# Performance work log

Measured on AMD Instinct MI355X. Metric: run time of the kernel, lower is better.

Reference implementation:

```python
import jax, jax.numpy as jnp
import numpy as np
import math

H, G, DQK, DV = 16, 4, 64, 128  # n_head, n_kv_group, qk head dim, v head dim


def _rope(t):
    # t: [B, n, T, d] -- standard rotate-half RoPE, base 10000
    B, n, T, d = t.shape
    inv = 1.0 / (10000.0 ** (jnp.arange(0, d, 2, dtype=jnp.float32) / d))  # [d/2]
    ang = jnp.arange(T, dtype=jnp.float32)[:, None] * inv[None, :]          # [T, d/2]
    cos = jnp.concatenate([jnp.cos(ang), jnp.cos(ang)], axis=-1)            # [T, d]
    sin = jnp.concatenate([jnp.sin(ang), jnp.sin(ang)], axis=-1)
    t1, t2 = jnp.split(t, 2, axis=-1)
    rot = jnp.concatenate([-t2, t1], axis=-1)
    return t * cos + rot * sin


def setup_inputs() -> dict:
    key = jax.random.key(0)
    ks = jax.random.split(key, 6)
    B, T, C = 2, 2048, 1024
    x = jax.random.normal(ks[0], (B, T, C), jnp.float32)
    Wq = jax.random.normal(ks[1], (C, H * DQK), jnp.float32) * 0.02
    Wk = jax.random.normal(ks[2], (C, G * DQK), jnp.float32) * 0.02
    Wv = jax.random.normal(ks[3], (C, G * DV), jnp.float32) * 0.02
    Wproj = jax.random.normal(ks[4], (DV, C), jnp.float32) * 0.02
    lobo = jnp.full((H,), 1.0, jnp.float32)  # flash_lobo_log_const per head
    g0 = math.log2(T * T - T)                # qk_norm_factor init from block_size
    qk_norm_factor = jnp.array([g0], dtype=jnp.float32)
    return {"x": x, "iter_num": 0, "Wq": Wq, "Wk": Wk, "Wv": Wv,
            "Wproj": Wproj, "lobo": lobo, "qk_norm_factor": qk_norm_factor}


def reference(x, iter_num, Wq, Wk, Wv, Wproj, lobo, qk_norm_factor):
    B, T, C = x.shape
    # projections (bias=False)
    q = (x @ Wq).reshape(B, T, H, DQK).transpose(0, 2, 1, 3)   # [B,H,T,dqk]
    k = (x @ Wk).reshape(B, T, G, DQK).transpose(0, 2, 1, 3)   # [B,G,T,dqk]
    v = (x @ Wv).reshape(B, T, G, DV).transpose(0, 2, 1, 3)    # [B,G,T,dv]
    # rotary embeddings on q and k
    q = _rope(q)
    k = _rope(k)
    # qk-norm
    q = q / (jnp.linalg.norm(q, axis=-1, keepdims=True) + 1e-6)
    k = k / (jnp.linalg.norm(k, axis=-1, keepdims=True) + 1e-6)
    # learned logit scale: q *= g*sqrt(d), SDPA divides by sqrt(d) -> net scale g
    q = q * (qk_norm_factor[0] * jnp.sqrt(jnp.float32(DQK)))
    # GQA broadcast (repeat_interleave over kv groups)
    rep = H // G
    k = jnp.repeat(k, rep, axis=1)   # [B,H,T,dqk]
    v = jnp.repeat(v, rep, axis=1)   # [B,H,T,dv]
    logits = jnp.einsum('bhqd,bhkd->bhqk', q, k) / jnp.sqrt(jnp.float32(DQK))
    causal = jnp.tril(jnp.ones((T, T), dtype=bool))
    logits = jnp.where(causal[None, None], logits, -jnp.inf)
    # flash-lobo: zero-valued sink key, always visible, logit = per-head bias
    sink = jnp.broadcast_to(lobo[None, :, None, None], (B, H, T, 1))
    att = jax.nn.softmax(jnp.concatenate([sink, logits], axis=-1), axis=-1)
    y = jnp.einsum('bhqk,bhkd->bhqd', att[..., 1:], v)  # sink value is zero
    y = y.sum(axis=1)                                    # head-SUM merge [B,T,dv]
    return y @ Wproj                                     # [B,T,C]
```

## Files before the change

### kernel.cpp

```cpp
#include <hip/hip_runtime.h>
#include <hip/hip_bf16.h>
#include <math.h>

#define B_ 2
#define T_ 2048
#define C_ 1024
#define H_ 16
#define G_ 4
#define DQK_ 64
#define DV_ 128
#define NQKV 1792
#define KS2 2048

typedef __attribute__((ext_vector_type(8))) short short8;
typedef __attribute__((ext_vector_type(4))) float f32x4;
typedef unsigned short ushort_t;

__device__ inline ushort_t f2bf(float f) {
  union { float f; unsigned int u; } v; v.f = f;
  unsigned int r = (v.u + 0x7FFFu + ((v.u >> 16) & 1u)) >> 16;
  return (ushort_t)r;
}
__device__ inline float bf2f(ushort_t h) {
  union { unsigned int u; float f; } v; v.u = ((unsigned int)h) << 16;
  return v.f;
}
__device__ inline ushort_t f2bf_hw(float f) {
  unsigned int u;
  asm("v_cvt_pk_bf16_f32 %0, %1, %1" : "=v"(u) : "v"(f));
  return (ushort_t)u;
}

#define GLD_LDS16(g, l)                                              \
  __builtin_amdgcn_global_load_lds(                                  \
      (const __attribute__((address_space(1))) void*)(g),            \
      (__attribute__((address_space(3))) void*)(l), 16, 0, 0)

__global__ __launch_bounds__(256) void cast_x(
    const float* __restrict__ x, ushort_t* __restrict__ xb) {
  int idx = blockIdx.x * 256 + threadIdx.x;
  int m = idx >> 7;
  int c8 = idx & 127;
  const float* src = &x[(size_t)m * 1024 + c8 * 8];
  float4 v0 = *(const float4*)&src[0];
  float4 v1 = *(const float4*)&src[4];
  float f[8] = {v0.x, v0.y, v0.z, v0.w, v1.x, v1.y, v1.z, v1.w};
  short8 hv, lv;
#pragma unroll
  for (int c = 0; c < 8; c++) {
    ushort_t h = f2bf(f[c]);
    hv[c] = (short)h;
    lv[c] = (short)f2bf(f[c] - bf2f(h));
  }
  int key = (m >> 1) & 3;
  int phys = (c8 & ~3) * 8 + ((c8 & 3) ^ key) * 8;
  ushort_t* row = xb + (size_t)m * KS2;
  *(short8*)&row[phys] = hv;
  *(short8*)&row[1024 + phys] = lv;
}

__global__ __launch_bounds__(256) void cast_w(
    const float* __restrict__ Wq, const float* __restrict__ Wk,
    const float* __restrict__ Wv, ushort_t* __restrict__ wt) {
  __shared__ float tile[64][65];
  const int n0 = blockIdx.x * 64;
  const int k0 = blockIdx.y * 64;
  const int tid = threadIdx.x;

  const float* Wp; int ldw, noff;
  if (n0 < 1024)      { Wp = Wq; ldw = 1024; noff = n0; }
  else if (n0 < 1280) { Wp = Wk; ldw = 256;  noff = n0 - 1024; }
  else                { Wp = Wv; ldw = 512;  noff = n0 - 1280; }

#pragma unroll
  for (int it = 0; it < 4; it++) {
    int fi = it * 256 + tid;
    int kk = fi >> 4;
    int nc = (fi & 15) * 4;
    float4 v = *(const float4*)&Wp[(size_t)(k0 + kk) * ldw + noff + nc];
    tile[nc + 0][kk] = v.x; tile[nc + 1][kk] = v.y;
    tile[nc + 2][kk] = v.z; tile[nc + 3][kk] = v.w;
  }
  __syncthreads();
  int nn = tid >> 2, seg = tid & 3;
  int n = n0 + nn;
  int key = (n >> 1) & 3;
  ushort_t* row = wt + (size_t)n * KS2;
#pragma unroll
  for (int j = 0; j < 2; j++) {
    short8 hv;
#pragma unroll
    for (int u = 0; u < 8; u++)
      hv[u] = (short)f2bf(tile[nn][seg * 16 + j * 8 + u]);
    int c8 = (k0 >> 3) + seg * 2 + j;
    int phys = (c8 & ~3) * 8 + ((c8 & 3) ^ key) * 8;
    *(short8*)&row[phys] = hv;
  }
}

__global__ __launch_bounds__(256) void cast_wp(
    const float* __restrict__ Wp, ushort_t* __restrict__ wpf) {
  int idx = blockIdx.x * 256 + threadIdx.x;
  int n = idx & 1023;
  int kc = idx >> 10;
  short8 v;
#pragma unroll
  for (int j = 0; j < 8; j++)
    v[j] = (short)f2bf(Wp[(size_t)(kc * 8 + j) * 1024 + n]);
  size_t off = (((size_t)(n >> 7) * 4 + (kc >> 2)) * 8 + ((n >> 4) & 7)) * 512 +
               ((kc & 3) * 16 + (n & 15)) * 8;
  *(short8*)&wpf[off] = v;
}

__global__ __launch_bounds__(256) void gemm_qkv_mfma(
    const ushort_t* __restrict__ xb, const ushort_t* __restrict__ wt,
    float* __restrict__ qkv) {
  __shared__ ushort_t At[128 * 32];
  __shared__ ushort_t Bt[128 * 32];
  const int tid = threadIdx.x;
  const int wave = tid >> 6, lane = tid & 63;
  const int quad = lane >> 4, l16 = lane & 15;
  const int m0 = blockIdx.y * 128, n0 = blockIdx.x * 128;
  const int wm = (wave & 1) * 64, wn = (wave >> 1) * 64;
  const int physq = (quad ^ ((l16 >> 1) & 3)) * 8;
  const int ntiles = (n0 >= 1280) ? 32 : 64;

  f32x4 acc[4][4];
#pragma unroll
  for (int i = 0; i < 4; i++)
#pragma unroll
    for (int j = 0; j < 4; j++) acc[i][j] = (f32x4){0.f, 0.f, 0.f, 0.f};

  const int rA = wave * 32 + (lane >> 2);
  const int cA = (lane & 3) * 8;
  const ushort_t* gA = xb + (size_t)(m0 + rA) * KS2 + cA;
  const ushort_t* gB = wt + (size_t)(n0 + rA) * KS2 + cA;
  ushort_t* lA0 = At + (size_t)(wave * 32) * 32;
  ushort_t* lA1 = At + (size_t)(wave * 32 + 16) * 32;
  ushort_t* lB0 = Bt + (size_t)(wave * 32) * 32;
  ushort_t* lB1 = Bt + (size_t)(wave * 32 + 16) * 32;

  for (int kt = 0; kt < ntiles; kt++) {
    const int ca = kt * 32;
    const int cb = (kt < 32 ? kt : kt - 32) * 32;
    __syncthreads();
    GLD_LDS16(gA + ca, lA0);
    GLD_LDS16(gA + ca + 16 * KS2, lA1);
    GLD_LDS16(gB + cb, lB0);
    GLD_LDS16(gB + cb + 16 * KS2, lB1);
    __syncthreads();

    short8 af[4], bf[4];
#pragma unroll
    for (int i = 0; i < 4; i++)
      af[i] = *(const short8*)&At[(wm + 16 * i + l16) * 32 + physq];
#pragma unroll
    for (int j = 0; j < 4; j++)
      bf[j] = *(const short8*)&Bt[(wn + 16 * j + l16) * 32 + physq];
#pragma unroll
    for (int i = 0; i < 4; i++)
#pragma unroll
      for (int j = 0; j < 4; j++)
        acc[i][j] = __builtin_amdgcn_mfma_f32_16x16x32_bf16(
            af[i], bf[j], acc[i][j], 0, 0, 0);
  }

#pragma unroll
  for (int i = 0; i < 4; i++) {
    int m = m0 + wm + 16 * i + quad * 4;
#pragma unroll
    for (int j = 0; j < 4; j++) {
      int n = n0 + wn + 16 * j + l16;
#pragma unroll
      for (int r = 0; r < 4; r++)
        qkv[(size_t)(m + r) * NQKV + n] = acc[i][j][r];
    }
  }
}

__global__ __launch_bounds__(256) void rope_norm(
    const float* __restrict__ qkv,
    ushort_t* __restrict__ qf, ushort_t* __restrict__ kf) {
  const int NQ = B_ * T_ * H_;
  int vec = blockIdx.x * 4 + (threadIdx.x >> 6);
  int d = threadIdx.x & 63;

  size_t src; int t, b, isq; ushort_t* dstbase;
  if (vec < NQ) {
    int h = vec % H_; int bt = vec / H_;
    t = bt % T_; b = bt / T_;
    src = (size_t)bt * NQKV + h * 64 + d;
    dstbase = qf + (size_t)(b * 16 + h) * 131072;
    isq = 1;
  } else {
    int vk = vec - NQ;
    int g = vk % G_; int bt = vk / G_;
    t = bt % T_; b = bt / T_;
    src = (size_t)bt * NQKV + 1024 + g * 64 + d;
    dstbase = kf + (size_t)(b * 4 + g) * 131072;
    isq = 0;
  }
  float val = qkv[src];
  int i = d & 31;
  float inv = exp2f(-(float)i * 0.4152410118074239f);
  float ang = (float)t * inv;
  float sn, cs;
  __sincosf(ang, &sn, &cs);
  float partner = __shfl(val, d ^ 32, 64);
  float r = (d < 32) ? (val * cs - partner * sn) : (val * cs + partner * sn);
  float ss = r * r;
#pragma unroll
  for (int off = 32; off; off >>= 1) ss += __shfl_xor(ss, off, 64);
  r *= 1.0f / (sqrtf(ss) + 1e-6f);

  int kt = t >> 6, tt = t & 63;
  int l16v = tt & 15;
  int ks = d >> 5, quad = (d >> 3) & 3, j = d & 7;
  size_t off2;
  if (isq) {
    int wavei = tt >> 4;
    off2 = ((size_t)(kt * 8 + wavei * 2 + ks) * 4 + quad) * 128 + l16v * 8 + j;
  } else {
    int nt = tt >> 4;
    off2 = ((size_t)(kt * 8 + ks * 4 + nt) * 4 + quad) * 128 + l16v * 8 + j;
  }
  dstbase[off2] = f2bf(r);
}

__global__ __launch_bounds__(256) void vscatter(
    const float* __restrict__ qkv, ushort_t* __restrict__ vf) {
  int idx = blockIdx.x * 256 + threadIdx.x;
  int dv = idx & 127;
  int t = (idx >> 7) & 2047;
  int g = (idx >> 18) & 3;
  int b = idx >> 20;
  size_t src = (size_t)(b * T_ + t) * NQKV + 1280 + g * 128 + dv;
  float v = qkv[src];
  int kt = t >> 6, ks = (t >> 5) & 1, quad = (t >> 3) & 3, j = t & 7;
  int nv = dv >> 4, l16v = dv & 15;
  size_t off = ((size_t)(kt * 16 + ks * 8 + nv) * 4 + quad) * 128 + l16v * 8 + j;
  vf[(size_t)(b * 4 + g) * 262144 + off] = f2bf(v);
}

__global__ __launch_bounds__(256, 4) void attn(
    const ushort_t* __restrict__ qf, const ushort_t* __restrict__ kf,
    const ushort_t* __restrict__ vf, const float* __restrict__ lobo,
    const float* __restrict__ qknf, float* __restrict__ y) {
  const int f = blockIdx.x;
  const int bh = f & 31;
  const int slot = f >> 5;
  int tq;
  if (slot < 8)       tq = 31 - slot;
  else if (slot < 16) tq = 8 + slot;
  else if (slot < 24) tq = 31 - slot;
  else                tq = slot - 24;
  const int b = bh >> 4;
  const int h = bh & 15;
  const int g = h >> 2;

  __shared__ ushort_t KV[12288];
  __shared__ ushort_t Ps[4 * 1088];

  const int tid = threadIdx.x;
  const int wave = tid >> 6, lane = tid & 63;
  const int quad = lane >> 4, l16 = lane & 15;
  ushort_t* PsW = &Ps[wave * 1088];

  short8 bones;
  {
    short bv = (l16 == 0) ? (short)0x3F80 : (short)0;
#pragma unroll
    for (int j = 0; j < 8; j++) bones[j] = bv;
  }

  const ushort_t* qbase = qf + (size_t)(b * 16 + h) * 131072 + lane * 8;
  short8 aq0 = *(const short8*)&qbase[(size_t)(tq * 8 + wave * 2 + 0) * 512];
  short8 aq1 = *(const short8*)&qbase[(size_t)(tq * 8 + wave * 2 + 1) * 512];

  f32x4 o[9];
#pragma unroll
  for (int nv = 0; nv < 9; nv++) o[nv] = (f32x4){0.f, 0.f, 0.f, 0.f};

  const float gsc = qknf[0];
  const float sinkp = __expf(lobo[h] - gsc);

  const int row = tq * 64 + wave * 16 + quad * 4;

  const ushort_t* kgl = kf + (size_t)(b * 4 + g) * 131072 + lane * 8;
  const ushort_t* vgl = vf + (size_t)(b * 4 + g) * 262144 + lane * 8;

  for (int kt = 0; kt <= tq; kt++) {
    __syncthreads();
    {
      const ushort_t* gk = kgl + (size_t)kt * 4096;
      const ushort_t* gv = vgl + (size_t)kt * 8192;
      GLD_LDS16(gk + (wave * 2 + 0) * 512, &KV[(wave * 2 + 0) * 512]);
      GLD_LDS16(gk + (wave * 2 + 1) * 512, &KV[(wave * 2 + 1) * 512]);
#pragma unroll
      for (int j = 0; j < 4; j++)
        GLD_LDS16(gv + (wave * 4 + j) * 512, &KV[4096 + (wave * 4 + j) * 512]);
    }
    __syncthreads();

    f32x4 s[4];
#pragma unroll
    for (int nt = 0; nt < 4; nt++) s[nt] = (f32x4){0.f, 0.f, 0.f, 0.f};
    {
      short8 kb[4];
#pragma unroll
      for (int u = 0; u < 4; u++)
        kb[u] = *(const short8*)&KV[u * 512 + lane * 8];
      __builtin_amdgcn_s_setprio(1);
#pragma unroll
      for (int nt = 0; nt < 4; nt++)
        s[nt] = __builtin_amdgcn_mfma_f32_16x16x32_bf16(aq0, kb[nt], s[nt], 0, 0, 0);
      __builtin_amdgcn_s_setprio(0);
#pragma unroll
      for (int u = 0; u < 4; u++)
        kb[u] = *(const short8*)&KV[(4 + u) * 512 + lane * 8];
      __builtin_amdgcn_s_setprio(1);
#pragma unroll
      for (int nt = 0; nt < 4; nt++)
        s[nt] = __builtin_amdgcn_mfma_f32_16x16x32_bf16(aq1, kb[nt], s[nt], 0, 0, 0);
      __builtin_amdgcn_s_setprio(0);
    }

    if (kt == tq) {
#pragma unroll
      for (int nt = 0; nt < 4; nt++) {
        int key = kt * 64 + l16 + nt * 16;
#pragma unroll
        for (int r = 0; r < 4; r++) {
          float pv = (key <= row + r) ? __expf(fmaf(s[nt][r], gsc, -gsc)) : 0.f;
          PsW[(quad * 4 + r) * 68 + nt * 16 + l16] = f2bf_hw(pv);
        }
      }
    } else {
#pragma unroll
      for (int nt = 0; nt < 4; nt++)
#pragma unroll
        for (int r = 0; r < 4; r++)
          PsW[(quad * 4 + r) * 68 + nt * 16 + l16] =
              f2bf_hw(__expf(fmaf(s[nt][r], gsc, -gsc)));
    }

    short8 ap0 = *(const short8*)&PsW[l16 * 68 + quad * 8];
    short8 ap1 = *(const short8*)&PsW[l16 * 68 + 32 + quad * 8];
    {
      short8 vb[4];
#pragma unroll
      for (int u = 0; u < 4; u++)
        vb[u] = *(const short8*)&KV[4096 + u * 512 + lane * 8];
      __builtin_amdgcn_s_setprio(1);
#pragma unroll
      for (int nv = 0; nv < 4; nv++)
        o[nv] = __builtin_amdgcn_mfma_f32_16x16x32_bf16(ap0, vb[nv], o[nv], 0, 0, 0);
      __builtin_amdgcn_s_setprio(0);
#pragma unroll
      for (int u = 0; u < 4; u++)
        vb[u] = *(const short8*)&KV[4096 + (4 + u) * 512 + lane * 8];
      __builtin_amdgcn_s_setprio(1);
#pragma unroll
      for (int nv = 0; nv < 4; nv++)
        o[4 + nv] = __builtin_amdgcn_mfma_f32_16x16x32_bf16(ap0, vb[nv], o[4 + nv], 0, 0, 0);
      o[8] = __builtin_amdgcn_mfma_f32_16x16x32_bf16(ap0, bones, o[8], 0, 0, 0);
      o[8] = __builtin_amdgcn_mfma_f32_16x16x32_bf16(ap1, bones, o[8], 0, 0, 0);
      __builtin_amdgcn_s_setprio(0);
#pragma unroll
      for (int u = 0; u < 4; u++)
        vb[u] = *(const short8*)&KV[4096 + (8 + u) * 512 + lane * 8];
      __builtin_amdgcn_s_setprio(1);
#pragma unroll
      for (int nv = 0; nv < 4; nv++)
        o[nv] = __builtin_amdgcn_mfma_f32_16x16x32_bf16(ap1, vb[nv], o[nv], 0, 0, 0);
      __builtin_amdgcn_s_setprio(0);
#pragma unroll
      for (int u = 0; u < 4; u++)
        vb[u] = *(const short8*)&KV[4096 + (12 + u) * 512 + lane * 8];
      __builtin_amdgcn_s_setprio(1);
#pragma unroll
      for (int nv = 0; nv < 4; nv++)
        o[4 + nv] = __builtin_amdgcn_mfma_f32_16x16x32_bf16(ap1, vb[nv], o[4 + nv], 0, 0, 0);
      __builtin_amdgcn_s_setprio(0);
    }
  }

#pragma unroll
  for (int r = 0; r < 4; r++) {
    float lm = __shfl(o[8][r], lane & 48, 64);
    float invl = 1.0f / (lm + sinkp);
    size_t gRow = (size_t)b * T_ + row + r;
#pragma unroll
    for (int nv = 0; nv < 8; nv++)
      atomicAdd(&y[gRow * 128 + nv * 16 + l16], o[nv][r] * invl);
  }
}

__global__ __launch_bounds__(256) void out_proj(
    const float* __restrict__ y, const ushort_t* __restrict__ wpf,
    float* __restrict__ out) {
  __shared__ ushort_t yl[128 * 136];
  const int tid = threadIdx.x;
  const int wave = tid >> 6, lane = tid & 63;
  const int quad = lane >> 4, l16 = lane & 15;
  const int n0 = blockIdx.x * 128, m0 = blockIdx.y * 128;
  const int wm = (wave & 1) * 64, wn = (wave >> 1) * 64;

#pragma unroll
  for (int it = 0; it < 8; it++) {
    int p = it * 256 + tid;
    int row = p >> 4, c8 = p & 15;
    const float* src = &y[(size_t)(m0 + row) * 128 + c8 * 8];
    float4 v0 = *(const float4*)&src[0];
    float4 v1 = *(const float4*)&src[4];
    float fv[8] = {v0.x, v0.y, v0.z, v0.w, v1.x, v1.y, v1.z, v1.w};
    short8 hv;
#pragma unroll
    for (int c = 0; c < 8; c++) hv[c] = (short)f2bf(fv[c]);
    *(short8*)&yl[row * 136 + c8 * 8] = hv;
  }
  __syncthreads();

  f32x4 acc[4][4];
#pragma unroll
  for (int i = 0; i < 4; i++)
#pragma unroll
    for (int j = 0; j < 4; j++) acc[i][j] = (f32x4){0.f, 0.f, 0.f, 0.f};

#pragma unroll
  for (int ks = 0; ks < 4; ks++) {
    short8 af[4], bfr[4];
#pragma unroll
    for (int i = 0; i < 4; i++)
      af[i] = *(const short8*)&yl[(wm + 16 * i + l16) * 136 + (ks * 4 + quad) * 8];
    const ushort_t* wb = wpf + (((size_t)(n0 >> 7) * 4 + ks) * 8) * 512;
#pragma unroll
    for (int j = 0; j < 4; j++)
      bfr[j] = *(const short8*)&wb[((size_t)((wn >> 4) + j)) * 512 + lane * 8];
#pragma unroll
    for (int i = 0; i < 4; i++)
#pragma unroll
      for (int j = 0; j < 4; j++)
        acc[i][j] = __builtin_amdgcn_mfma_f32_16x16x32_bf16(
            af[i], bfr[j], acc[i][j], 0, 0, 0);
  }

#pragma unroll
  for (int i = 0; i < 4; i++) {
    int m = m0 + wm + 16 * i + quad * 4;
#pragma unroll
    for (int j = 0; j < 4; j++) {
      int n = n0 + wn + 16 * j + l16;
#pragma unroll
      for (int r = 0; r < 4; r++)
        out[(size_t)(m + r) * 1024 + n] = acc[i][j][r];
    }
  }
}

extern "C" void kernel_launch(void* const* d_in, const int* in_sizes, int n_in,
                              void* d_out, int out_size, void* d_ws, size_t ws_size,
                              hipStream_t stream) {
  const float* x     = (const float*)d_in[0];
  const float* Wq    = (const float*)d_in[2];
  const float* Wk    = (const float*)d_in[3];
  const float* Wv    = (const float*)d_in[4];
  const float* Wproj = (const float*)d_in[5];
  const float* lobo  = (const float*)d_in[6];
  const float* qknf  = (const float*)d_in[7];
  float* out = (float*)d_out;

  float* qkv = (float*)d_ws;
  ushort_t* xb = (ushort_t*)(qkv + (size_t)B_ * T_ * NQKV);
  ushort_t* wt = xb + (size_t)B_ * T_ * KS2;
  ushort_t* wpf = wt + (size_t)NQKV * KS2;
  ushort_t* qf = xb;
  ushort_t* kf = qf + (size_t)B_ * H_ * T_ * 64;
  ushort_t* vf = kf + (size_t)B_ * G_ * T_ * 64;
  float* y = (float*)(vf + (size_t)B_ * G_ * T_ * 128);

  cast_x<<<(B_ * T_ * 128) / 256, 256, 0, stream>>>(x, xb);
  dim3 gw(NQKV / 64, C_ / 64);
  cast_w<<<gw, 256, 0, stream>>>(Wq, Wk, Wv, wt);
  cast_wp<<<64, 256, 0, stream>>>(Wproj, wpf);

  dim3 gg(NQKV / 128, (B_ * T_) / 128);
  gemm_qkv_mfma<<<gg, 256, 0, stream>>>(xb, wt, qkv);

  int nvec = B_ * T_ * H_ + B_ * T_ * G_;
  rope_norm<<<nvec / 4, 256, 0, stream>>>(qkv, qf, kf);

  vscatter<<<(B_ * G_ * T_ * DV_) / 256, 256, 0, stream>>>(qkv, vf);

  (void)hipMemsetAsync(y, 0, (size_t)B_ * T_ * 128 * sizeof(float), stream);

  attn<<<B_ * H_ * 32, 256, 0, stream>>>(qf, kf, vf, lobo, qknf, y);

  dim3 go(8, 32);
  out_proj<<<go, 256, 0, stream>>>(y, wpf, out);
}
```

Before: 240.6 us.

## Double-buffer K tiles and overlap V loads with QK compute in attention

Splits the shared K/V tile into a double-buffered K buffer and a separate V buffer. Each iteration now issues the V load for the current tile and the K prefetch for the next tile, then runs the QK MFMAs while those loads are in flight, and only waits at a barrier placed before the PV stage. The goal is to hide global-to-LDS load latency behind the score computation. The extra LDS lowers the occupancy hint from 4 to 3 blocks, and the query-tile schedule becomes plain longest-first. The barrier before PV also waits on the next-K prefetch, so the overlap covers only the QK phase.

```diff
diff --git a/kernel.cpp b/kernel.cpp
--- a/kernel.cpp
+++ b/kernel.cpp
@@ -242,23 +242,20 @@
   vf[(size_t)(b * 4 + g) * 262144 + off] = f2bf(v);
 }
 
-__global__ __launch_bounds__(256, 4) void attn(
+__global__ __launch_bounds__(256, 3) void attn(
     const ushort_t* __restrict__ qf, const ushort_t* __restrict__ kf,
     const ushort_t* __restrict__ vf, const float* __restrict__ lobo,
     const float* __restrict__ qknf, float* __restrict__ y) {
   const int f = blockIdx.x;
   const int bh = f & 31;
   const int slot = f >> 5;
-  int tq;
-  if (slot < 8)       tq = 31 - slot;
-  else if (slot < 16) tq = 8 + slot;
-  else if (slot < 24) tq = 31 - slot;
-  else                tq = slot - 24;
+  const int tq = 31 - slot;
   const int b = bh >> 4;
   const int h = bh & 15;
   const int g = h >> 2;
 
-  __shared__ ushort_t KV[12288];
+  __shared__ ushort_t Kb[2][4096];
+  __shared__ ushort_t Vb[8192];
   __shared__ ushort_t Ps[4 * 1088];
 
   const int tid = threadIdx.x;
@@ -289,19 +286,25 @@
   const ushort_t* kgl = kf + (size_t)(b * 4 + g) * 131072 + lane * 8;
   const ushort_t* vgl = vf + (size_t)(b * 4 + g) * 262144 + lane * 8;
 
+  GLD_LDS16(kgl + (wave * 2 + 0) * 512, &Kb[0][(wave * 2 + 0) * 512]);
+  GLD_LDS16(kgl + (wave * 2 + 1) * 512, &Kb[0][(wave * 2 + 1) * 512]);
+  __syncthreads();
+
   for (int kt = 0; kt <= tq; kt++) {
-    __syncthreads();
     {
-      const ushort_t* gk = kgl + (size_t)kt * 4096;
       const ushort_t* gv = vgl + (size_t)kt * 8192;
-      GLD_LDS16(gk + (wave * 2 + 0) * 512, &KV[(wave * 2 + 0) * 512]);
-      GLD_LDS16(gk + (wave * 2 + 1) * 512, &KV[(wave * 2 + 1) * 512]);
 #pragma unroll
       for (int j = 0; j < 4; j++)
-        GLD_LDS16(gv + (wave * 4 + j) * 512, &KV[4096 + (wave * 4 + j) * 512]);
+        GLD_LDS16(gv + (wave * 4 + j) * 512, &Vb[(wave * 4 + j) * 512]);
+      if (kt < tq) {
+        const ushort_t* gk = kgl + (size_t)(kt + 1) * 4096;
+        ushort_t* kd = &Kb[(kt + 1) & 1][0];
+        GLD_LDS16(gk + (wave * 2 + 0) * 512, &kd[(wave * 2 + 0) * 512]);
+        GLD_LDS16(gk + (wave * 2 + 1) * 512, &kd[(wave * 2 + 1) * 512]);
+      }
     }
-    __syncthreads();
-
+
+    const ushort_t* Kc = &Kb[kt & 1][0];
     f32x4 s[4];
 #pragma unroll
     for (int nt = 0; nt < 4; nt++) s[nt] = (f32x4){0.f, 0.f, 0.f, 0.f};
@@ -309,7 +312,7 @@
       short8 kb[4];
 #pragma unroll
       for (int u = 0; u < 4; u++)
-        kb[u] = *(const short8*)&KV[u * 512 + lane * 8];
+        kb[u] = *(const short8*)&Kc[u * 512 + lane * 8];
       __builtin_amdgcn_s_setprio(1);
 #pragma unroll
       for (int nt = 0; nt < 4; nt++)
@@ -317,7 +320,7 @@
       __builtin_amdgcn_s_setprio(0);
 #pragma unroll
       for (int u = 0; u < 4; u++)
-        kb[u] = *(const short8*)&KV[(4 + u) * 512 + lane * 8];
+        kb[u] = *(const short8*)&Kc[(4 + u) * 512 + lane * 8];
       __builtin_amdgcn_s_setprio(1);
 #pragma unroll
       for (int nt = 0; nt < 4; nt++)
@@ -344,13 +347,15 @@
               f2bf_hw(__expf(fmaf(s[nt][r], gsc, -gsc)));
     }
 
+    __syncthreads();
+
     short8 ap0 = *(const short8*)&PsW[l16 * 68 + quad * 8];
     short8 ap1 = *(const short8*)&PsW[l16 * 68 + 32 + quad * 8];
     {
       short8 vb[4];
 #pragma unroll
       for (int u = 0; u < 4; u++)
-        vb[u] = *(const short8*)&KV[4096 + u * 512 + lane * 8];
+        vb[u] = *(const short8*)&Vb[u * 512 + lane * 8];
       __builtin_amdgcn_s_setprio(1);
 #pragma unroll
       for (int nv = 0; nv < 4; nv++)
@@ -358,7 +363,7 @@
       __builtin_amdgcn_s_setprio(0);
 #pragma unroll
       for (int u = 0; u < 4; u++)
-        vb[u] = *(const short8*)&KV[4096 + (4 + u) * 512 + lane * 8];
+        vb[u] = *(const short8*)&Vb[(4 + u) * 512 + lane * 8];
       __builtin_amdgcn_s_setprio(1);
 #pragma unroll
       for (int nv = 0; nv < 4; nv++)
@@ -368,7 +373,7 @@
       __builtin_amdgcn_s_setprio(0);
 #pragma unroll
       for (int u = 0; u < 4; u++)
-        vb[u] = *(const short8*)&KV[4096 + (8 + u) * 512 + lane * 8];
+        vb[u] = *(const short8*)&Vb[(8 + u) * 512 + lane * 8];
       __builtin_amdgcn_s_setprio(1);
 #pragma unroll
       for (int nv = 0; nv < 4; nv++)
@@ -376,13 +381,15 @@
       __builtin_amdgcn_s_setprio(0);
 #pragma unroll
       for (int u = 0; u < 4; u++)
-        vb[u] = *(const short8*)&KV[4096 + (12 + u) * 512 + lane * 8];
+        vb[u] = *(const short8*)&Vb[(12 + u) * 512 + lane * 8];
       __builtin_amdgcn_s_setprio(1);
 #pragma unroll
       for (int nv = 0; nv < 4; nv++)
         o[4 + nv] = __builtin_amdgcn_mfma_f32_16x16x32_bf16(ap1, vb[nv], o[4 + nv], 0, 0, 0);
       __builtin_amdgcn_s_setprio(0);
     }
+
+    __syncthreads();
   }
 
 #pragma unroll
```

Measured after the change: 243.6 us. About the same (+1.2%).

## Merge prep casts and rope/scatter/memset into single launches; widen GEMM K-tile

Applied to the files above, without the earlier changes.

Combines the three weight/activation cast kernels into one block-indexed prep kernel, and the rope-norm, V scatter and y zeroing memset into one rope_scatter kernel. Together this cuts four kernel launches and their inter-kernel gaps. The QKV GEMM now stages 64-wide K tiles per barrier pair instead of 32, using larger LDS buffers. That halves the number of synchronizations per output tile and issues more async loads per barrier. The cost is more shared memory per block and branchy combined kernels.

```diff
diff --git a/kernel.cpp b/kernel.cpp
--- a/kernel.cpp
+++ b/kernel.cpp
@@ -36,94 +36,95 @@
       (const __attribute__((address_space(1))) void*)(g),            \
       (__attribute__((address_space(3))) void*)(l), 16, 0, 0)
 
-__global__ __launch_bounds__(256) void cast_x(
-    const float* __restrict__ x, ushort_t* __restrict__ xb) {
-  int idx = blockIdx.x * 256 + threadIdx.x;
-  int m = idx >> 7;
-  int c8 = idx & 127;
-  const float* src = &x[(size_t)m * 1024 + c8 * 8];
-  float4 v0 = *(const float4*)&src[0];
-  float4 v1 = *(const float4*)&src[4];
-  float f[8] = {v0.x, v0.y, v0.z, v0.w, v1.x, v1.y, v1.z, v1.w};
-  short8 hv, lv;
-#pragma unroll
-  for (int c = 0; c < 8; c++) {
-    ushort_t h = f2bf(f[c]);
-    hv[c] = (short)h;
-    lv[c] = (short)f2bf(f[c] - bf2f(h));
-  }
-  int key = (m >> 1) & 3;
-  int phys = (c8 & ~3) * 8 + ((c8 & 3) ^ key) * 8;
-  ushort_t* row = xb + (size_t)m * KS2;
-  *(short8*)&row[phys] = hv;
-  *(short8*)&row[1024 + phys] = lv;
-}
-
-__global__ __launch_bounds__(256) void cast_w(
-    const float* __restrict__ Wq, const float* __restrict__ Wk,
-    const float* __restrict__ Wv, ushort_t* __restrict__ wt) {
+__global__ __launch_bounds__(256) void prep(
+    const float* __restrict__ x, const float* __restrict__ Wq,
+    const float* __restrict__ Wk, const float* __restrict__ Wv,
+    const float* __restrict__ Wproj, ushort_t* __restrict__ xb,
+    ushort_t* __restrict__ wt, ushort_t* __restrict__ wpf) {
   __shared__ float tile[64][65];
-  const int n0 = blockIdx.x * 64;
-  const int k0 = blockIdx.y * 64;
+  const int bid = blockIdx.x;
   const int tid = threadIdx.x;
 
-  const float* Wp; int ldw, noff;
-  if (n0 < 1024)      { Wp = Wq; ldw = 1024; noff = n0; }
-  else if (n0 < 1280) { Wp = Wk; ldw = 256;  noff = n0 - 1024; }
-  else                { Wp = Wv; ldw = 512;  noff = n0 - 1280; }
-
-#pragma unroll
-  for (int it = 0; it < 4; it++) {
-    int fi = it * 256 + tid;
-    int kk = fi >> 4;
-    int nc = (fi & 15) * 4;
-    float4 v = *(const float4*)&Wp[(size_t)(k0 + kk) * ldw + noff + nc];
-    tile[nc + 0][kk] = v.x; tile[nc + 1][kk] = v.y;
-    tile[nc + 2][kk] = v.z; tile[nc + 3][kk] = v.w;
-  }
-  __syncthreads();
-  int nn = tid >> 2, seg = tid & 3;
-  int n = n0 + nn;
-  int key = (n >> 1) & 3;
-  ushort_t* row = wt + (size_t)n * KS2;
-#pragma unroll
-  for (int j = 0; j < 2; j++) {
-    short8 hv;
-#pragma unroll
-    for (int u = 0; u < 8; u++)
-      hv[u] = (short)f2bf(tile[nn][seg * 16 + j * 8 + u]);
-    int c8 = (k0 >> 3) + seg * 2 + j;
+  if (bid < 2048) {
+    int idx = bid * 256 + tid;
+    int m = idx >> 7;
+    int c8 = idx & 127;
+    const float* src = &x[(size_t)m * 1024 + c8 * 8];
+    float4 v0 = *(const float4*)&src[0];
+    float4 v1 = *(const float4*)&src[4];
+    float f[8] = {v0.x, v0.y, v0.z, v0.w, v1.x, v1.y, v1.z, v1.w};
+    short8 hv, lv;
+#pragma unroll
+    for (int c = 0; c < 8; c++) {
+      ushort_t h = f2bf(f[c]);
+      hv[c] = (short)h;
+      lv[c] = (short)f2bf(f[c] - bf2f(h));
+    }
+    int key = (m >> 1) & 3;
     int phys = (c8 & ~3) * 8 + ((c8 & 3) ^ key) * 8;
+    ushort_t* row = xb + (size_t)m * KS2;
     *(short8*)&row[phys] = hv;
-  }
-}
-
-__global__ __launch_bounds__(256) void cast_wp(
-    const float* __restrict__ Wp, ushort_t* __restrict__ wpf) {
-  int idx = blockIdx.x * 256 + threadIdx.x;
-  int n = idx & 1023;
-  int kc = idx >> 10;
-  short8 v;
-#pragma unroll
-  for (int j = 0; j < 8; j++)
-    v[j] = (short)f2bf(Wp[(size_t)(kc * 8 + j) * 1024 + n]);
-  size_t off = (((size_t)(n >> 7) * 4 + (kc >> 2)) * 8 + ((n >> 4) & 7)) * 512 +
-               ((kc & 3) * 16 + (n & 15)) * 8;
-  *(short8*)&wpf[off] = v;
+    *(short8*)&row[1024 + phys] = lv;
+  } else if (bid < 2496) {
+    const int wid = bid - 2048;
+    const int n0 = (wid % 28) * 64;
+    const int k0 = (wid / 28) * 64;
+
+    const float* Wp; int ldw, noff;
+    if (n0 < 1024)      { Wp = Wq; ldw = 1024; noff = n0; }
+    else if (n0 < 1280) { Wp = Wk; ldw = 256;  noff = n0 - 1024; }
+    else                { Wp = Wv; ldw = 512;  noff = n0 - 1280; }
+
+#pragma unroll
+    for (int it = 0; it < 4; it++) {
+      int fi = it * 256 + tid;
+      int kk = fi >> 4;
+      int nc = (fi & 15) * 4;
+      float4 v = *(const float4*)&Wp[(size_t)(k0 + kk) * ldw + noff + nc];
+      tile[nc + 0][kk] = v.x; tile[nc + 1][kk] = v.y;
+      tile[nc + 2][kk] = v.z; tile[nc + 3][kk] = v.w;
+    }
+    __syncthreads();
+    int nn = tid >> 2, seg = tid & 3;
+    int n = n0 + nn;
+    int key = (n >> 1) & 3;
+    ushort_t* row = wt + (size_t)n * KS2;
+#pragma unroll
+    for (int j = 0; j < 2; j++) {
+      short8 hv;
+#pragma unroll
+      for (int u = 0; u < 8; u++)
+        hv[u] = (short)f2bf(tile[nn][seg * 16 + j * 8 + u]);
+      int c8 = (k0 >> 3) + seg * 2 + j;
+      int phys = (c8 & ~3) * 8 + ((c8 & 3) ^ key) * 8;
+      *(short8*)&row[phys] = hv;
+    }
+  } else {
+    int idx = (bid - 2496) * 256 + tid;
+    int n = idx & 1023;
+    int kc = idx >> 10;
+    short8 v;
+#pragma unroll
+    for (int j = 0; j < 8; j++)
+      v[j] = (short)f2bf(Wproj[(size_t)(kc * 8 + j) * 1024 + n]);
+    size_t off = (((size_t)(n >> 7) * 4 + (kc >> 2)) * 8 + ((n >> 4) & 7)) * 512 +
+                 ((kc & 3) * 16 + (n & 15)) * 8;
+    *(short8*)&wpf[off] = v;
+  }
 }
 
 __global__ __launch_bounds__(256) void gemm_qkv_mfma(
     const ushort_t* __restrict__ xb, const ushort_t* __restrict__ wt,
     float* __restrict__ qkv) {
-  __shared__ ushort_t At[128 * 32];
-  __shared__ ushort_t Bt[128 * 32];
+  __shared__ ushort_t At[128 * 64];
+  __shared__ ushort_t Bt[128 * 64];
   const int tid = threadIdx.x;
   const int wave = tid >> 6, lane = tid & 63;
   const int quad = lane >> 4, l16 = lane & 15;
   const int m0 = blockIdx.y * 128, n0 = blockIdx.x * 128;
   const int wm = (wave & 1) * 64, wn = (wave >> 1) * 64;
-  const int physq = (quad ^ ((l16 >> 1) & 3)) * 8;
-  const int ntiles = (n0 >= 1280) ? 32 : 64;
+  const int key = (l16 >> 1) & 3;
+  const int ntiles = (n0 >= 1280) ? 16 : 32;
 
   f32x4 acc[4][4];
 #pragma unroll
@@ -131,38 +132,39 @@
 #pragma unroll
     for (int j = 0; j < 4; j++) acc[i][j] = (f32x4){0.f, 0.f, 0.f, 0.f};
 
-  const int rA = wave * 32 + (lane >> 2);
-  const int cA = (lane & 3) * 8;
+  const int rA = wave * 32 + (lane >> 3);
+  const int cA = (lane & 7) * 8;
   const ushort_t* gA = xb + (size_t)(m0 + rA) * KS2 + cA;
   const ushort_t* gB = wt + (size_t)(n0 + rA) * KS2 + cA;
-  ushort_t* lA0 = At + (size_t)(wave * 32) * 32;
-  ushort_t* lA1 = At + (size_t)(wave * 32 + 16) * 32;
-  ushort_t* lB0 = Bt + (size_t)(wave * 32) * 32;
-  ushort_t* lB1 = Bt + (size_t)(wave * 32 + 16) * 32;
 
   for (int kt = 0; kt < ntiles; kt++) {
-    const int ca = kt * 32;
-    const int cb = (kt < 32 ? kt : kt - 32) * 32;
+    const int ca = kt * 64;
+    const int cb = (kt < 16 ? kt : kt - 16) * 64;
     __syncthreads();
-    GLD_LDS16(gA + ca, lA0);
-    GLD_LDS16(gA + ca + 16 * KS2, lA1);
-    GLD_LDS16(gB + cb, lB0);
-    GLD_LDS16(gB + cb + 16 * KS2, lB1);
+#pragma unroll
+    for (int j = 0; j < 4; j++) {
+      GLD_LDS16(gA + ca + (size_t)(8 * j) * KS2, &At[(wave * 32 + 8 * j) * 64]);
+      GLD_LDS16(gB + cb + (size_t)(8 * j) * KS2, &Bt[(wave * 32 + 8 * j) * 64]);
+    }
     __syncthreads();
 
-    short8 af[4], bf[4];
-#pragma unroll
-    for (int i = 0; i < 4; i++)
-      af[i] = *(const short8*)&At[(wm + 16 * i + l16) * 32 + physq];
-#pragma unroll
-    for (int j = 0; j < 4; j++)
-      bf[j] = *(const short8*)&Bt[(wn + 16 * j + l16) * 32 + physq];
-#pragma unroll
-    for (int i = 0; i < 4; i++)
+#pragma unroll
+    for (int s = 0; s < 2; s++) {
+      const int off = s * 32 + ((quad ^ key) * 8);
+      short8 af[4], bf[4];
+#pragma unroll
+      for (int i = 0; i < 4; i++)
+        af[i] = *(const short8*)&At[(wm + 16 * i + l16) * 64 + off];
 #pragma unroll
       for (int j = 0; j < 4; j++)
-        acc[i][j] = __builtin_amdgcn_mfma_f32_16x16x32_bf16(
-            af[i], bf[j], acc[i][j], 0, 0, 0);
+        bf[j] = *(const short8*)&Bt[(wn + 16 * j + l16) * 64 + off];
+#pragma unroll
+      for (int i = 0; i < 4; i++)
+#pragma unroll
+        for (int j = 0; j < 4; j++)
+          acc[i][j] = __builtin_amdgcn_mfma_f32_16x16x32_bf16(
+              af[i], bf[j], acc[i][j], 0, 0, 0);
+    }
   }
 
 #pragma unroll
@@ -178,68 +180,74 @@
   }
 }
 
-__global__ __launch_bounds__(256) void rope_norm(
-    const float* __restrict__ qkv,
-    ushort_t* __restrict__ qf, ushort_t* __restrict__ kf) {
-  const int NQ = B_ * T_ * H_;
-  int vec = blockIdx.x * 4 + (threadIdx.x >> 6);
-  int d = threadIdx.x & 63;
-
-  size_t src; int t, b, isq; ushort_t* dstbase;
-  if (vec < NQ) {
-    int h = vec % H_; int bt = vec / H_;
-    t = bt % T_; b = bt / T_;
-    src = (size_t)bt * NQKV + h * 64 + d;
-    dstbase = qf + (size_t)(b * 16 + h) * 131072;
-    isq = 1;
+__global__ __launch_bounds__(256) void rope_scatter(
+    const float* __restrict__ qkv, ushort_t* __restrict__ qf,
+    ushort_t* __restrict__ kf, ushort_t* __restrict__ vf,
+    float* __restrict__ y) {
+  const int bid = blockIdx.x;
+  const int tid = threadIdx.x;
+
+  if (bid < 20480) {
+    const int NQ = B_ * T_ * H_;
+    int vec = bid * 4 + (tid >> 6);
+    int d = tid & 63;
+
+    size_t src; int t, b, isq; ushort_t* dstbase;
+    if (vec < NQ) {
+      int h = vec % H_; int bt = vec / H_;
+      t = bt % T_; b = bt / T_;
+      src = (size_t)bt * NQKV + h * 64 + d;
+      dstbase = qf + (size_t)(b * 16 + h) * 131072;
+      isq = 1;
+    } else {
+      int vk = vec - NQ;
+      int g = vk % G_; int bt = vk / G_;
+      t = bt % T_; b = bt / T_;
+      src = (size_t)bt * NQKV + 1024 + g * 64 + d;
+      dstbase = kf + (size_t)(b * 4 + g) * 131072;
+      isq = 0;
+    }
+    float val = qkv[src];
+    int i = d & 31;
+    float inv = exp2f(-(float)i * 0.4152410118074239f);
+    float ang = (float)t * inv;
+    float sn, cs;
+    __sincosf(ang, &sn, &cs);
+    float partner = __shfl(val, d ^ 32, 64);
+    float r = (d < 32) ? (val * cs - partner * sn) : (val * cs + partner * sn);
+    float ss = r * r;
+#pragma unroll
+    for (int off = 32; off; off >>= 1) ss += __shfl_xor(ss, off, 64);
+    r *= 1.0f / (sqrtf(ss) + 1e-6f);
+
+    int kt = t >> 6, tt = t & 63;
+    int l16v = tt & 15;
+    int ks = d >> 5, quad = (d >> 3) & 3, j = d & 7;
+    size_t off2;
+    if (isq) {
+      int wavei = tt >> 4;
+      off2 = ((size_t)(kt * 8 + wavei * 2 + ks) * 4 + quad) * 128 + l16v * 8 + j;
+    } else {
+      int nt = tt >> 4;
+      off2 = ((size_t)(kt * 8 + ks * 4 + nt) * 4 + quad) * 128 + l16v * 8 + j;
+    }
+    dstbase[off2] = f2bf(r);
+  } else if (bid < 28672) {
+    int idx = (bid - 20480) * 256 + tid;
+    int dv = idx & 127;
+    int t = (idx >> 7) & 2047;
+    int g = (idx >> 18) & 3;
+    int b = idx >> 20;
+    size_t src = (size_t)(b * T_ + t) * NQKV + 1280 + g * 128 + dv;
+    float v = qkv[src];
+    int kt = t >> 6, ks = (t >> 5) & 1, quad = (t >> 3) & 3, j = t & 7;
+    int nv = dv >> 4, l16v = dv & 15;
+    size_t off = ((size_t)(kt * 16 + ks * 8 + nv) * 4 + quad) * 128 + l16v * 8 + j;
+    vf[(size_t)(b * 4 + g) * 262144 + off] = f2bf(v);
   } else {
-    int vk = vec - NQ;
-    int g = vk % G_; int bt = vk / G_;
-    t = bt % T_; b = bt / T_;
-    src = (size_t)bt * NQKV + 1024 + g * 64 + d;
-    dstbase = kf + (size_t)(b * 4 + g) * 131072;
-    isq = 0;
-  }
-  float val = qkv[src];
-  int i = d & 31;
-  float inv = exp2f(-(float)i * 0.4152410118074239f);
-  float ang = (float)t * inv;
-  float sn, cs;
-  __sincosf(ang, &sn, &cs);
-  float partner = __shfl(val, d ^ 32, 64);
-  float r = (d < 32) ? (val * cs - partner * sn) : (val * cs + partner * sn);
-  float ss = r * r;
-#pragma unroll
-  for (int off = 32; off; off >>= 1) ss += __shfl_xor(ss, off, 64);
-  r *= 1.0f / (sqrtf(ss) + 1e-6f);
-
-  int kt = t >> 6, tt = t & 63;
-  int l16v = tt & 15;
-  int ks = d >> 5, quad = (d >> 3) & 3, j = d & 7;
-  size_t off2;
-  if (isq) {
-    int wavei = tt >> 4;
-    off2 = ((size_t)(kt * 8 + wavei * 2 + ks) * 4 + quad) * 128 + l16v * 8 + j;
-  } else {
-    int nt = tt >> 4;
-    off2 = ((size_t)(kt * 8 + ks * 4 + nt) * 4 + quad) * 128 + l16v * 8 + j;
-  }
-  dstbase[off2] = f2bf(r);
-}
-
-__global__ __launch_bounds__(256) void vscatter(
-    const float* __restrict__ qkv, ushort_t* __restrict__ vf) {
-  int idx = blockIdx.x * 256 + threadIdx.x;
-  int dv = idx & 127;
-  int t = (idx >> 7) & 2047;
-  int g = (idx >> 18) & 3;
-  int b = idx >> 20;
-  size_t src = (size_t)(b * T_ + t) * NQKV + 1280 + g * 128 + dv;
-  float v = qkv[src];
-  int kt = t >> 6, ks = (t >> 5) & 1, quad = (t >> 3) & 3, j = t & 7;
-  int nv = dv >> 4, l16v = dv & 15;
-  size_t off = ((size_t)(kt * 16 + ks * 8 + nv) * 4 + quad) * 128 + l16v * 8 + j;
-  vf[(size_t)(b * 4 + g) * 262144 + off] = f2bf(v);
+    int idx = (bid - 28672) * 256 + tid;
+    *(float4*)&y[(size_t)idx * 4] = (float4){0.f, 0.f, 0.f, 0.f};
+  }
 }
 
 __global__ __launch_bounds__(256, 4) void attn(
@@ -479,20 +487,12 @@
   ushort_t* vf = kf + (size_t)B_ * G_ * T_ * 64;
   float* y = (float*)(vf + (size_t)B_ * G_ * T_ * 128);
 
-  cast_x<<<(B_ * T_ * 128) / 256, 256, 0, stream>>>(x, xb);
-  dim3 gw(NQKV / 64, C_ / 64);
-  cast_w<<<gw, 256, 0, stream>>>(Wq, Wk, Wv, wt);
-  cast_wp<<<64, 256, 0, stream>>>(Wproj, wpf);
+  prep<<<2560, 256, 0, stream>>>(x, Wq, Wk, Wv, Wproj, xb, wt, wpf);
 
   dim3 gg(NQKV / 128, (B_ * T_) / 128);
   gemm_qkv_mfma<<<gg, 256, 0, stream>>>(xb, wt, qkv);
 
-  int nvec = B_ * T_ * H_ + B_ * T_ * G_;
-  rope_norm<<<nvec / 4, 256, 0, stream>>>(qkv, qf, kf);
-
-  vscatter<<<(B_ * G_ * T_ * DV_) / 256, 256, 0, stream>>>(qkv, vf);
-
-  (void)hipMemsetAsync(y, 0, (size_t)B_ * T_ * 128 * sizeof(float), stream);
+  rope_scatter<<<29184, 256, 0, stream>>>(qkv, qf, kf, vf, y);
 
   attn<<<B_ * H_ * 32, 256, 0, stream>>>(qf, kf, vf, lobo, qknf, y);
 
```

Result: faster. 216.3 us (-10.1%).
